# Optimization experiments

Measured on AMD Instinct MI355X. Metric: run time of the kernel, lower is better.

## Reference

```python
import jax, jax.numpy as jnp
import numpy as np

HID = 128

def _sage(h, src, dst, Wl, bl, Wr, n):
    # PyG SAGEConv (mean aggr): out = lin_l(mean_{j in N(i)} h_j) + lin_r(h_i)
    msg = h[src]                                   # [E, H] gather
    s = jax.ops.segment_sum(msg, dst, num_segments=n)
    cnt = jax.ops.segment_sum(jnp.ones_like(dst, dtype=h.dtype), dst, num_segments=n)
    m = s / jnp.maximum(cnt, 1.0)[:, None]
    return m @ Wl + bl + h @ Wr

def setup_inputs() -> dict:
    key = jax.random.key(0)
    ks = jax.random.split(key, 20)
    NP, NC, E = 20000, 80000, 1600000
    N = NP + NC
    inp = {
        'x_pol_dyn': jax.random.normal(ks[0], (NP, 64), jnp.float32),
        'pol_state_idx': jax.random.randint(ks[1], (NP,), 0, 50),
        'x_comp_dyn': jax.random.normal(ks[2], (NC, 96), jnp.float32),
        'comp_sector_idx': jax.random.randint(ks[3], (NC,), 0, 12),
        'comp_ind_idx': jax.random.randint(ks[4], (NC,), 0, 150),
        'edge_index': jax.random.randint(ks[5], (2, E), 0, N),
        'state_emb': jax.random.normal(ks[6], (50, 8), jnp.float32) * 0.1,
        'sector_emb': jax.random.normal(ks[7], (12, 8), jnp.float32) * 0.1,
        'ind_emb': jax.random.normal(ks[8], (150, 8), jnp.float32) * 0.1,
        'W_pol': jax.random.normal(ks[9], (64 + 8, HID), jnp.float32) * 0.05,
        'b_pol': jnp.zeros((HID,), jnp.float32),
        'W_comp': jax.random.normal(ks[10], (96 + 16, HID), jnp.float32) * 0.05,
        'b_comp': jnp.zeros((HID,), jnp.float32),
        'Wl1': jax.random.normal(ks[11], (HID, HID), jnp.float32) * 0.05,
        'bl1': jnp.zeros((HID,), jnp.float32),
        'Wr1': jax.random.normal(ks[12], (HID, HID), jnp.float32) * 0.05,
        'Wl2': jax.random.normal(ks[13], (HID, HID), jnp.float32) * 0.05,
        'bl2': jnp.zeros((HID,), jnp.float32),
        'Wr2': jax.random.normal(ks[14], (HID, HID), jnp.float32) * 0.05,
    }
    return inp

def reference(x_pol_dyn, pol_state_idx, x_comp_dyn, comp_sector_idx, comp_ind_idx,
              edge_index, state_emb, sector_emb, ind_emb,
              W_pol, b_pol, W_comp, b_comp, Wl1, bl1, Wr1, Wl2, bl2, Wr2):
    pol_feat = jnp.concatenate([x_pol_dyn, state_emb[pol_state_idx]], axis=-1)
    comp_feat = jnp.concatenate([x_comp_dyn, sector_emb[comp_sector_idx], ind_emb[comp_ind_idx]], axis=-1)
    h_pol = jax.nn.relu(pol_feat @ W_pol + b_pol)
    h_comp = jax.nn.relu(comp_feat @ W_comp + b_comp)
    # dropout is identity in eval mode
    h = jnp.concatenate([h_pol, h_comp], axis=0)
    n = h.shape[0]
    src, dst = edge_index[0], edge_index[1]
    h = jax.nn.relu(_sage(h, src, dst, Wl1, bl1, Wr1, n))
    h = _sage(h, src, dst, Wl2, bl2, Wr2, n)
    np_ = h_pol.shape[0]
    return h[:np_], h[np_:]
```

## Files before the change

kernel.cpp:

```cpp
#include <hip/hip_runtime.h>

#define NP 20000
#define NC 80000
#define NN 100000
#define NE 1600000
#define HD 128
#define MAXDEG 64
#define BKT 391
#define BINB 391

typedef unsigned short ushort_t;
typedef unsigned int uint_t;

typedef __attribute__((ext_vector_type(8))) short bf16x8;
typedef __attribute__((ext_vector_type(4))) float f32x4;

__device__ __forceinline__ ushort_t f2bf(float f) {
  uint_t u = __builtin_bit_cast(uint_t, f);
  u = (u + 0x7FFF + ((u >> 16) & 1)) >> 16;
  return (ushort_t)u;
}
__device__ __forceinline__ float bf_lo(uint_t p) {
  return __builtin_bit_cast(float, p << 16);
}
__device__ __forceinline__ float bf_hi(uint_t p) {
  return __builtin_bit_cast(float, p & 0xFFFF0000u);
}
__device__ __forceinline__ uint4 pack8(float4 lo, float4 hi) {
  ushort_t t[8];
  t[0] = f2bf(lo.x); t[1] = f2bf(lo.y); t[2] = f2bf(lo.z); t[3] = f2bf(lo.w);
  t[4] = f2bf(hi.x); t[5] = f2bf(hi.y); t[6] = f2bf(hi.z); t[7] = f2bf(hi.w);
  return *(uint4*)t;
}

__device__ __forceinline__ void pack_tile(const float* __restrict__ W,
                                          ushort_t* __restrict__ P, int KF,
                                          int KB, int task) {
  int t = task / (KB * 64);
  int rem = task - t * KB * 64;
  int kb = rem >> 6;
  int lane = rem & 63;
  int k0 = kb * 32 + ((lane >> 4) << 3);
  int c = t * 16 + (lane & 15);
  ushort_t tmp[8];
#pragma unroll
  for (int j = 0; j < 8; ++j) {
    int k = k0 + j;
    tmp[j] = (k < KF) ? f2bf(W[(size_t)k * HD + c]) : (ushort_t)0;
  }
  *(uint4*)(P + (size_t)task * 8) = *(uint4*)tmp;
}

#define PACKB 46
__global__ __launch_bounds__(256) void prep_k(
    const int* __restrict__ dst, int* __restrict__ bcnt,
    const float* __restrict__ Wl1, const float* __restrict__ Wr1,
    const float* __restrict__ Wl2, const float* __restrict__ Wr2,
    const float* __restrict__ W_comp, const float* __restrict__ W_pol,
    ushort_t* __restrict__ wl1p, ushort_t* __restrict__ wr1p,
    ushort_t* __restrict__ wl2p, ushort_t* __restrict__ wr2p,
    ushort_t* __restrict__ wcompp, ushort_t* __restrict__ wpolp) {
  __shared__ int hist[BKT];
  int blk = blockIdx.x;
  int tid = threadIdx.x;
  if (blk < BINB) {
    for (int t = tid; t < BKT; t += 256) hist[t] = 0;
    __syncthreads();
    int base = blk * 4096;
#pragma unroll
    for (int q = 0; q < 16; ++q) {
      int e = base + q * 256 + tid;
      if (e < NE) atomicAdd(&hist[dst[e] >> 8], 1);
    }
    __syncthreads();
    for (int t = tid; t < BKT; t += 256)
      if (hist[t] > 0) atomicAdd(&bcnt[t], hist[t]);
    return;
  }
  int pb = blk - BINB;
  if (pb < 8) pack_tile(Wl1, wl1p, 128, 4, pb * 256 + tid);
  else if (pb < 16) pack_tile(Wr1, wr1p, 128, 4, (pb - 8) * 256 + tid);
  else if (pb < 24) pack_tile(Wl2, wl2p, 128, 4, (pb - 16) * 256 + tid);
  else if (pb < 32) pack_tile(Wr2, wr2p, 128, 4, (pb - 24) * 256 + tid);
  else if (pb < 40) pack_tile(W_comp, wcompp, 112, 4, (pb - 32) * 256 + tid);
  else pack_tile(W_pol, wpolp, 72, 3, (pb - 40) * 256 + tid);
}

__global__ __launch_bounds__(512) void scan_k(const int* __restrict__ bcnt,
                                              int* __restrict__ bstart,
                                              int* __restrict__ bfill) {
  __shared__ int s[512];
  int t = threadIdx.x;
  int v = (t < BKT) ? bcnt[t] : 0;
  s[t] = v;
  __syncthreads();
  for (int off = 1; off < 512; off <<= 1) {
    int x = (t >= off) ? s[t - off] : 0;
    __syncthreads();
    s[t] += x;
    __syncthreads();
  }
  if (t < BKT) {
    int st = s[t] - v;
    bstart[t] = st;
    bfill[t] = st;
  }
}

#define COMP_E (NC / 128)
#define POL_E ((NP + 127) / 128)
__global__ __launch_bounds__(512) void bin_enc_k(
    const int* __restrict__ src, const int* __restrict__ dst,
    int* __restrict__ bfill, uint_t* __restrict__ ebuf,
    const float* __restrict__ x_comp, const int* __restrict__ sec,
    const int* __restrict__ ind, const float* __restrict__ semb,
    const float* __restrict__ iemb, const ushort_t* __restrict__ wcompp,
    const float* __restrict__ b_comp,
    const float* __restrict__ x_pol, const int* __restrict__ sidx,
    const float* __restrict__ stemb, const ushort_t* __restrict__ wpolp,
    const float* __restrict__ b_pol,
    ushort_t* __restrict__ h0) {
  __shared__ int hist[BKT];
  __shared__ int lscan[BKT];
  __shared__ int gbase[BKT];
  __shared__ int sv[512];
  __shared__ uint2 stage[4096];
  int blk = blockIdx.x;
  int tid = threadIdx.x;

  if (blk < BINB) {
    for (int t = tid; t < BKT; t += 512) hist[t] = 0;
    __syncthreads();
    int base = blk * 4096;
    int cntE = min(4096, NE - base);
    int ss[8], dd[8], rr[8];
#pragma unroll
    for (int q = 0; q < 8; ++q) {
      int e = base + q * 512 + tid;
      if (e < NE) {
        dd[q] = dst[e];
        ss[q] = src[e];
        rr[q] = atomicAdd(&hist[dd[q] >> 8], 1);
      } else {
        dd[q] = -1;
      }
    }
    __syncthreads();
    int hv = (tid < BKT) ? hist[tid] : 0;
    sv[tid] = hv;
    __syncthreads();
    for (int off = 1; off < 512; off <<= 1) {
      int x = (tid >= off) ? sv[tid - off] : 0;
      __syncthreads();
      sv[tid] += x;
      __syncthreads();
    }
    if (tid < BKT) {
      lscan[tid] = sv[tid] - hv;
      if (hv > 0) gbase[tid] = atomicAdd(&bfill[tid], hv);
    }
    __syncthreads();
#pragma unroll
    for (int q = 0; q < 8; ++q) {
      if (dd[q] >= 0) {
        int bb = dd[q] >> 8;
        stage[lscan[bb] + rr[q]] = make_uint2((uint_t)ss[q], (uint_t)dd[q]);
      }
    }
    __syncthreads();
    for (int j = tid; j < cntE; j += 512) {
      uint2 v = stage[j];
      int bb = v.y >> 8;
      ebuf[gbase[bb] + (j - lscan[bb])] = (v.x << 8) | (v.y & 255u);
    }
    return;
  }
  int lane = tid & 63;
  int wv = tid >> 6;
  int n16 = lane & 15, quad = lane >> 4;
  if (blk < BINB + COMP_E) {
    int rowbase = (blk - BINB) * 128 + wv * 16;
    int node = rowbase + n16;
    const float4* xr = (const float4*)(x_comp + (size_t)node * 96);
    uint4 a[4];
#pragma unroll
    for (int kb = 0; kb < 3; ++kb)
      a[kb] = pack8(xr[kb * 8 + quad * 2], xr[kb * 8 + quad * 2 + 1]);
    if (quad == 0) {
      const float4* er = (const float4*)(semb + (size_t)sec[node] * 8);
      a[3] = pack8(er[0], er[1]);
    } else if (quad == 1) {
      const float4* er = (const float4*)(iemb + (size_t)ind[node] * 8);
      a[3] = pack8(er[0], er[1]);
    } else {
      a[3] = make_uint4(0, 0, 0, 0);
    }
    const bf16x8* W = (const bf16x8*)wcompp;
    ushort_t* hb = h0 + (size_t)NP * HD;
#pragma unroll
    for (int t = 0; t < 8; ++t) {
      float bias = b_comp[t * 16 + n16];
      f32x4 acc = {bias, bias, bias, bias};
#pragma unroll
      for (int kb = 0; kb < 4; ++kb)
        acc = __builtin_amdgcn_mfma_f32_16x16x32_bf16(
            __builtin_bit_cast(bf16x8, a[kb]), W[(t * 4 + kb) * 64 + lane],
            acc, 0, 0, 0);
      int r0 = rowbase + quad * 4;
      int c = t * 16 + n16;
#pragma unroll
      for (int r = 0; r < 4; ++r)
        hb[(size_t)(r0 + r) * HD + c] = f2bf(fmaxf(acc[r], 0.f));
    }
    return;
  }
  {
    int rowbase = (blk - BINB - COMP_E) * 128 + wv * 16;
    if (rowbase >= NP) return;
    int node = rowbase + n16;
    const float4* xr = (const float4*)(x_pol + (size_t)node * 64);
    uint4 a[3];
#pragma unroll
    for (int kb = 0; kb < 2; ++kb)
      a[kb] = pack8(xr[kb * 8 + quad * 2], xr[kb * 8 + quad * 2 + 1]);
    if (quad == 0) {
      const float4* er = (const float4*)(stemb + (size_t)sidx[node] * 8);
      a[2] = pack8(er[0], er[1]);
    } else {
      a[2] = make_uint4(0, 0, 0, 0);
    }
    const bf16x8* W = (const bf16x8*)wpolp;
#pragma unroll
    for (int t = 0; t < 8; ++t) {
      float bias = b_pol[t * 16 + n16];
      f32x4 acc = {bias, bias, bias, bias};
#pragma unroll
      for (int kb = 0; kb < 3; ++kb)
        acc = __builtin_amdgcn_mfma_f32_16x16x32_bf16(
            __builtin_bit_cast(bf16x8, a[kb]), W[(t * 3 + kb) * 64 + lane],
            acc, 0, 0, 0);
      int r0 = rowbase + quad * 4;
      int c = t * 16 + n16;
#pragma unroll
      for (int r = 0; r < 4; ++r)
        h0[(size_t)(r0 + r) * HD + c] = f2bf(fmaxf(acc[r], 0.f));
    }
  }
}

__global__ __launch_bounds__(512) void build_k(const uint_t* __restrict__ ebuf,
                                               const int* __restrict__ bstart,
                                               const int* __restrict__ bcnt,
                                               int* __restrict__ col,
                                               int* __restrict__ cnt) {
  __shared__ int lcnt[256];
  int tid = threadIdx.x;
  int b = blockIdx.x;
  if (tid < 256) lcnt[tid] = 0;
  __syncthreads();
  int st = bstart[b];
  int cb = bcnt[b];
  for (int off = tid; off < cb; off += 512) {
    uint_t v = ebuf[st + off];
    int nl = v & 255u;
    int p = atomicAdd(&lcnt[nl], 1);
    if (p < MAXDEG) col[(size_t)((b << 8) | nl) * MAXDEG + p] = (int)(v >> 8);
  }
  __syncthreads();
  if (tid < 256) {
    int node = (b << 8) + tid;
    if (node < NN) cnt[node] = lcnt[tid];
  }
}

__global__ __launch_bounds__(256) void aggregate_k(
    const ushort_t* __restrict__ hbf, const int* __restrict__ cnt,
    const int* __restrict__ col, ushort_t* __restrict__ mbf) {
  const uint4* hrow = (const uint4*)hbf;
  int lane = threadIdx.x & 63;
  int i = blockIdx.x * 4 + (threadIdx.x >> 6);
  int d = min(cnt[i], MAXDEG);
  int grp = lane >> 4;
  int l16 = lane & 15;
  float acc[8] = {0.f, 0.f, 0.f, 0.f, 0.f, 0.f, 0.f, 0.f};
  int myc = (lane < d) ? col[(size_t)i * MAXDEG + lane] : 0;
  int nch = (d + 15) >> 4;
  for (int ch = 0; ch < nch; ++ch) {
    int j0 = ch * 16;
    uint4 p[4];
    bool v[4];
#pragma unroll
    for (int q = 0; q < 4; ++q) {
      int e = j0 + q * 4 + grp;
      v[q] = e < d;
      int s = __shfl(myc, v[q] ? e : 0);
      p[q] = hrow[(size_t)s * 16 + l16];
    }
#pragma unroll
    for (int q = 0; q < 4; ++q) {
      if (v[q]) {
        acc[0] += bf_lo(p[q].x); acc[1] += bf_hi(p[q].x);
        acc[2] += bf_lo(p[q].y); acc[3] += bf_hi(p[q].y);
        acc[4] += bf_lo(p[q].z); acc[5] += bf_hi(p[q].z);
        acc[6] += bf_lo(p[q].w); acc[7] += bf_hi(p[q].w);
      }
    }
  }
#pragma unroll
  for (int k = 0; k < 8; ++k) {
    acc[k] += __shfl_xor(acc[k], 16);
    acc[k] += __shfl_xor(acc[k], 32);
  }
  float inv = 1.f / (float)max(d, 1);
  if (grp == 0) {
    ushort_t t[8];
#pragma unroll
    for (int k = 0; k < 8; ++k) t[k] = f2bf(acc[k] * inv);
    *(uint4*)(mbf + (size_t)i * HD + l16 * 8) = *(uint4*)t;
  }
}

__global__ __launch_bounds__(256) void sage_mfma_k(
    const ushort_t* __restrict__ mb, const ushort_t* __restrict__ hb,
    const ushort_t* __restrict__ Wlp, const float* __restrict__ bl,
    const ushort_t* __restrict__ Wrp, float* __restrict__ outf,
    ushort_t* __restrict__ outb, int relu) {
  int lane = threadIdx.x & 63;
  int rowbase = blockIdx.x * 64 + (threadIdx.x >> 6) * 16;
  if (rowbase >= NN) return;
  int n16 = lane & 15, quad = lane >> 4;
  const uint4* mrow = (const uint4*)(mb + (size_t)(rowbase + n16) * HD);
  const uint4* hrow = (const uint4*)(hb + (size_t)(rowbase + n16) * HD);
  uint4 am[4], ah[4];
#pragma unroll
  for (int kb = 0; kb < 4; ++kb) {
    am[kb] = mrow[kb * 4 + quad];
    ah[kb] = hrow[kb * 4 + quad];
  }
  const bf16x8* WL = (const bf16x8*)Wlp;
  const bf16x8* WR = (const bf16x8*)Wrp;
#pragma unroll
  for (int t = 0; t < 8; ++t) {
    float bias = bl[t * 16 + n16];
    f32x4 acc = {bias, bias, bias, bias};
#pragma unroll
    for (int kb = 0; kb < 4; ++kb)
      acc = __builtin_amdgcn_mfma_f32_16x16x32_bf16(
          __builtin_bit_cast(bf16x8, am[kb]), WL[(t * 4 + kb) * 64 + lane],
          acc, 0, 0, 0);
#pragma unroll
    for (int kb = 0; kb < 4; ++kb)
      acc = __builtin_amdgcn_mfma_f32_16x16x32_bf16(
          __builtin_bit_cast(bf16x8, ah[kb]), WR[(t * 4 + kb) * 64 + lane],
          acc, 0, 0, 0);
    int r0 = rowbase + quad * 4;
    int c = t * 16 + n16;
#pragma unroll
    for (int r = 0; r < 4; ++r) {
      float v = acc[r];
      if (relu) v = fmaxf(v, 0.f);
      if (outb)
        outb[(size_t)(r0 + r) * HD + c] = f2bf(v);
      else
        outf[(size_t)(r0 + r) * HD + c] = v;
    }
  }
}

extern "C" void kernel_launch(void* const* d_in, const int* in_sizes, int n_in,
                              void* d_out, int out_size, void* d_ws,
                              size_t ws_size, hipStream_t stream) {
  const float* x_pol = (const float*)d_in[0];
  const int* pol_state_idx = (const int*)d_in[1];
  const float* x_comp = (const float*)d_in[2];
  const int* comp_sector = (const int*)d_in[3];
  const int* comp_ind = (const int*)d_in[4];
  const int* edge = (const int*)d_in[5];
  const float* state_emb = (const float*)d_in[6];
  const float* sector_emb = (const float*)d_in[7];
  const float* ind_emb = (const float*)d_in[8];
  const float* W_pol = (const float*)d_in[9];
  const float* b_pol = (const float*)d_in[10];
  const float* W_comp = (const float*)d_in[11];
  const float* b_comp = (const float*)d_in[12];
  const float* Wl1 = (const float*)d_in[13];
  const float* bl1 = (const float*)d_in[14];
  const float* Wr1 = (const float*)d_in[15];
  const float* Wl2 = (const float*)d_in[16];
  const float* bl2 = (const float*)d_in[17];
  const float* Wr2 = (const float*)d_in[18];

  const int* src = edge;
  const int* dst = edge + NE;

  const size_t HBYTES = (size_t)NN * HD * sizeof(ushort_t);
  char* ws = (char*)d_ws;
  ushort_t* m_bf = (ushort_t*)ws;
  ushort_t* h0_bf = (ushort_t*)(ws + HBYTES);
  ushort_t* h1_bf = (ushort_t*)(ws + 2 * HBYTES);
  int* col = (int*)(ws + 3 * HBYTES);
  uint_t* ebuf = (uint_t*)(col + (size_t)NN * MAXDEG);
  int* cnt = (int*)(ebuf + NE);
  ushort_t* wl1p = (ushort_t*)(cnt + NN);
  ushort_t* wr1p = wl1p + 16384;
  ushort_t* wl2p = wr1p + 16384;
  ushort_t* wr2p = wl2p + 16384;
  ushort_t* wcompp = wr2p + 16384;
  ushort_t* wpolp = wcompp + 16384;
  int* bcnt = (int*)(wpolp + 12288);
  int* bstart = bcnt + BKT;
  int* bfill = bstart + BKT;

  float* out_f = (float*)d_out;

  hipMemsetAsync(bcnt, 0, BKT * sizeof(int), stream);

  prep_k<<<BINB + PACKB, 256, 0, stream>>>(dst, bcnt, Wl1, Wr1, Wl2, Wr2,
                                           W_comp, W_pol, wl1p, wr1p, wl2p,
                                           wr2p, wcompp, wpolp);
  scan_k<<<1, 512, 0, stream>>>(bcnt, bstart, bfill);
  bin_enc_k<<<BINB + COMP_E + POL_E, 512, 0, stream>>>(
      src, dst, bfill, ebuf, x_comp, comp_sector, comp_ind, sector_emb,
      ind_emb, wcompp, b_comp, x_pol, pol_state_idx, state_emb, wpolp, b_pol,
      h0_bf);
  build_k<<<BKT, 512, 0, stream>>>(ebuf, bstart, bcnt, col, cnt);

  const int GB = (NN + 63) / 64;
  aggregate_k<<<NN / 4, 256, 0, stream>>>(h0_bf, cnt, col, m_bf);
  sage_mfma_k<<<GB, 256, 0, stream>>>(m_bf, h0_bf, wl1p, bl1, wr1p, nullptr,
                                      h1_bf, 1);

  aggregate_k<<<NN / 4, 256, 0, stream>>>(h1_bf, cnt, col, m_bf);
  sage_mfma_k<<<GB, 256, 0, stream>>>(m_bf, h1_bf, wl2p, bl2, wr2p, out_f,
                                      nullptr, 0);
}
```

Measured before the change: 344.4 us.

## Fuse neighbor mean aggregation into SAGE MFMA kernel via LDS staging

Merges the aggregation kernel and the SAGE linear kernel into one. Each wave now aggregates its 16 rows one after another, stages the bf16 means in shared memory, and feeds them straight to the MFMA matmul. This removes the global m_bf round-trip and two launches per layer. In exchange each wave processes rows serially (with prefetch of the next row's column list), so there are far fewer waves in flight (1563 blocks vs 25000) to hide gather latency.

```diff
diff --git a/kernel.cpp b/kernel.cpp
--- a/kernel.cpp
+++ b/kernel.cpp
@@ -273,69 +273,73 @@
   }
 }
 
-__global__ __launch_bounds__(256) void aggregate_k(
+__global__ __launch_bounds__(256) void agg_sage_k(
     const ushort_t* __restrict__ hbf, const int* __restrict__ cnt,
-    const int* __restrict__ col, ushort_t* __restrict__ mbf) {
+    const int* __restrict__ col, const ushort_t* __restrict__ Wlp,
+    const float* __restrict__ bl, const ushort_t* __restrict__ Wrp,
+    float* __restrict__ outf, ushort_t* __restrict__ outb, int relu) {
+  __shared__ __align__(16) ushort_t lm[4][16][136];
   const uint4* hrow = (const uint4*)hbf;
   int lane = threadIdx.x & 63;
-  int i = blockIdx.x * 4 + (threadIdx.x >> 6);
-  int d = min(cnt[i], MAXDEG);
+  int wv = threadIdx.x >> 6;
+  int rowbase = blockIdx.x * 64 + wv * 16;
+  if (rowbase >= NN) return;
   int grp = lane >> 4;
   int l16 = lane & 15;
-  float acc[8] = {0.f, 0.f, 0.f, 0.f, 0.f, 0.f, 0.f, 0.f};
-  int myc = (lane < d) ? col[(size_t)i * MAXDEG + lane] : 0;
-  int nch = (d + 15) >> 4;
-  for (int ch = 0; ch < nch; ++ch) {
-    int j0 = ch * 16;
-    uint4 p[4];
-    bool v[4];
-#pragma unroll
-    for (int q = 0; q < 4; ++q) {
-      int e = j0 + q * 4 + grp;
-      v[q] = e < d;
-      int s = __shfl(myc, v[q] ? e : 0);
-      p[q] = hrow[(size_t)s * 16 + l16];
-    }
-#pragma unroll
-    for (int q = 0; q < 4; ++q) {
-      if (v[q]) {
-        acc[0] += bf_lo(p[q].x); acc[1] += bf_hi(p[q].x);
-        acc[2] += bf_lo(p[q].y); acc[3] += bf_hi(p[q].y);
-        acc[4] += bf_lo(p[q].z); acc[5] += bf_hi(p[q].z);
-        acc[6] += bf_lo(p[q].w); acc[7] += bf_hi(p[q].w);
+
+  int dv = min(cnt[rowbase + l16], MAXDEG);
+  int d0 = __shfl(dv, 0);
+  int myc = (lane < d0) ? col[(size_t)rowbase * MAXDEG + lane] : 0;
+  for (int t = 0; t < 16; ++t) {
+    int i = rowbase + t;
+    int d = __shfl(dv, t);
+    int dn = (t < 15) ? __shfl(dv, t + 1) : 0;
+    int mycn = (lane < dn) ? col[(size_t)(i + 1) * MAXDEG + lane] : 0;
+    float acc[8] = {0.f, 0.f, 0.f, 0.f, 0.f, 0.f, 0.f, 0.f};
+    int nch = (d + 15) >> 4;
+    for (int ch = 0; ch < nch; ++ch) {
+      int j0 = ch * 16;
+      uint4 p[4];
+      bool v[4];
+#pragma unroll
+      for (int q = 0; q < 4; ++q) {
+        int e = j0 + q * 4 + grp;
+        v[q] = e < d;
+        int s = __shfl(myc, v[q] ? e : 0);
+        p[q] = hrow[(size_t)s * 16 + l16];
       }
-    }
-  }
-#pragma unroll
-  for (int k = 0; k < 8; ++k) {
-    acc[k] += __shfl_xor(acc[k], 16);
-    acc[k] += __shfl_xor(acc[k], 32);
-  }
-  float inv = 1.f / (float)max(d, 1);
-  if (grp == 0) {
-    ushort_t t[8];
-#pragma unroll
-    for (int k = 0; k < 8; ++k) t[k] = f2bf(acc[k] * inv);
-    *(uint4*)(mbf + (size_t)i * HD + l16 * 8) = *(uint4*)t;
-  }
-}
-
-__global__ __launch_bounds__(256) void sage_mfma_k(
-    const ushort_t* __restrict__ mb, const ushort_t* __restrict__ hb,
-    const ushort_t* __restrict__ Wlp, const float* __restrict__ bl,
-    const ushort_t* __restrict__ Wrp, float* __restrict__ outf,
-    ushort_t* __restrict__ outb, int relu) {
-  int lane = threadIdx.x & 63;
-  int rowbase = blockIdx.x * 64 + (threadIdx.x >> 6) * 16;
-  if (rowbase >= NN) return;
-  int n16 = lane & 15, quad = lane >> 4;
-  const uint4* mrow = (const uint4*)(mb + (size_t)(rowbase + n16) * HD);
-  const uint4* hrow = (const uint4*)(hb + (size_t)(rowbase + n16) * HD);
+#pragma unroll
+      for (int q = 0; q < 4; ++q) {
+        if (v[q]) {
+          acc[0] += bf_lo(p[q].x); acc[1] += bf_hi(p[q].x);
+          acc[2] += bf_lo(p[q].y); acc[3] += bf_hi(p[q].y);
+          acc[4] += bf_lo(p[q].z); acc[5] += bf_hi(p[q].z);
+          acc[6] += bf_lo(p[q].w); acc[7] += bf_hi(p[q].w);
+        }
+      }
+    }
+#pragma unroll
+    for (int k = 0; k < 8; ++k) {
+      acc[k] += __shfl_xor(acc[k], 16);
+      acc[k] += __shfl_xor(acc[k], 32);
+    }
+    float inv = 1.f / (float)max(d, 1);
+    if (grp == 0) {
+      ushort_t tt[8];
+#pragma unroll
+      for (int k = 0; k < 8; ++k) tt[k] = f2bf(acc[k] * inv);
+      *(uint4*)&lm[wv][t][l16 * 8] = *(uint4*)tt;
+    }
+    myc = mycn;
+  }
+
+  int n16 = l16, quad = grp;
+  const uint4* hr = (const uint4*)(hbf + (size_t)(rowbase + n16) * HD);
   uint4 am[4], ah[4];
 #pragma unroll
   for (int kb = 0; kb < 4; ++kb) {
-    am[kb] = mrow[kb * 4 + quad];
-    ah[kb] = hrow[kb * 4 + quad];
+    am[kb] = *(const uint4*)&lm[wv][n16][(kb * 4 + quad) * 8];
+    ah[kb] = hr[kb * 4 + quad];
   }
   const bf16x8* WL = (const bf16x8*)Wlp;
   const bf16x8* WR = (const bf16x8*)Wrp;
@@ -395,7 +399,6 @@
 
   const size_t HBYTES = (size_t)NN * HD * sizeof(ushort_t);
   char* ws = (char*)d_ws;
-  ushort_t* m_bf = (ushort_t*)ws;
   ushort_t* h0_bf = (ushort_t*)(ws + HBYTES);
   ushort_t* h1_bf = (ushort_t*)(ws + 2 * HBYTES);
   int* col = (int*)(ws + 3 * HBYTES);
@@ -426,11 +429,8 @@
   build_k<<<BKT, 512, 0, stream>>>(ebuf, bstart, bcnt, col, cnt);
 
   const int GB = (NN + 63) / 64;
-  aggregate_k<<<NN / 4, 256, 0, stream>>>(h0_bf, cnt, col, m_bf);
-  sage_mfma_k<<<GB, 256, 0, stream>>>(m_bf, h0_bf, wl1p, bl1, wr1p, nullptr,
-                                      h1_bf, 1);
-
-  aggregate_k<<<NN / 4, 256, 0, stream>>>(h1_bf, cnt, col, m_bf);
-  sage_mfma_k<<<GB, 256, 0, stream>>>(m_bf, h1_bf, wl2p, bl2, wr2p, out_f,
-                                      nullptr, 0);
-}
+  agg_sage_k<<<GB, 256, 0, stream>>>(h0_bf, cnt, col, wl1p, bl1, wr1p,
+                                     nullptr, h1_bf, 1);
+  agg_sage_k<<<GB, 256, 0, stream>>>(h1_bf, cnt, col, wl2p, bl2, wr2p, out_f,
+                                     nullptr, 0);
+}
```

After: 357.1 us. +3.7%, slower.
